# Kernel tuning notes

Measured on AMD Instinct MI355X. Metric: run time of the kernel, lower is better.

Reference implementation:

```python
import jax, jax.numpy as jnp
import numpy as np

B, L, D = 1, 2048, 768
H, DH = 12, 64  # n_heads, d_head (D // H)
LN_EPS = 1e-5
DEN_EPS = 1e-6


def setup_inputs() -> dict:
    key = jax.random.key(0)
    ks = jax.random.split(key, 11)
    s = 0.02
    return {
        "x": jax.random.normal(ks[0], (B, L, D), dtype=jnp.float32),
        "W_qkv": jax.random.normal(ks[1], (D, 3 * D), dtype=jnp.float32) * s,
        "b_qkv": jnp.zeros((3 * D,), dtype=jnp.float32),
        "W_sem": jax.random.normal(ks[2], (D, 2 * D), dtype=jnp.float32) * s,
        "b_sem": jnp.zeros((2 * D,), dtype=jnp.float32),
        "W_ctx": jax.random.normal(ks[3], (D, 2 * D), dtype=jnp.float32) * s,
        "b_ctx": jnp.zeros((2 * D,), dtype=jnp.float32),
        "W_proj": jax.random.normal(ks[4], (D, D), dtype=jnp.float32) * s,
        "b_proj": jnp.zeros((D,), dtype=jnp.float32),
        "ln_g": jnp.ones((D,), dtype=jnp.float32),
        "ln_b": jnp.zeros((D,), dtype=jnp.float32),
    }


def _heads(t):
    # [B,L,D] -> [B,H,L,DH]
    return t.reshape(B, L, H, DH).transpose(0, 2, 1, 3)


def reference(x, W_qkv, b_qkv, W_sem, b_sem, W_ctx, b_ctx, W_proj, b_proj, ln_g, ln_b):
    # LayerNorm
    mu = jnp.mean(x, axis=-1, keepdims=True)
    var = jnp.mean(jnp.square(x - mu), axis=-1, keepdims=True)
    x_norm = (x - mu) * jax.lax.rsqrt(var + LN_EPS) * ln_g + ln_b

    qkv = x_norm @ W_qkv + b_qkv
    q, k, v = jnp.split(qkv, 3, axis=-1)

    # interference gate from raw x
    sem = x @ W_sem + b_sem
    sem_amp = jax.nn.softplus(sem[..., :D])
    sem_phase = sem[..., D:]
    ctx = x @ W_ctx + b_ctx
    ctx_amp = jax.nn.softplus(ctx[..., :D])
    ctx_phase = ctx[..., D:]
    gate = jax.nn.sigmoid(sem_amp * ctx_amp * jnp.cos(sem_phase - ctx_phase))
    k = k * gate

    q_f = jax.nn.elu(_heads(q)) + 1.0  # [B,H,L,DH]
    k_f = jax.nn.elu(_heads(k)) + 1.0
    v_f = _heads(v)

    # causal linear attention: cumsum of kv outer products along L
    kv = jnp.einsum("bhld,bhle->bhlde", k_f, v_f)  # [B,H,L,DH,DH]
    kv_cum = jnp.cumsum(kv, axis=2)
    out_num = jnp.einsum("bhld,bhlde->bhle", q_f, kv_cum)  # [B,H,L,DH]

    k_cum = jnp.cumsum(k_f, axis=2)
    out_den = jnp.sum(q_f * k_cum, axis=-1, keepdims=True) + DEN_EPS

    attn = (out_num / out_den).transpose(0, 2, 1, 3).reshape(B, L, D)
    return attn @ W_proj + b_proj
```

## Files before the change

### kernel.cpp

```cpp
#include <hip/hip_runtime.h>
#include <math.h>

#define LSEQ 2048
#define DMODEL 768
#define NHEAD 12
#define DHEAD 64
#define NCHUNK 32
#define NMERGED 5376

typedef unsigned short ushort_t;
typedef __attribute__((ext_vector_type(8))) short short8;
typedef float float4v __attribute__((ext_vector_type(4)));

__device__ __forceinline__ ushort_t f2b(float f) {
    union { float f; unsigned int u; } v; v.f = f;
    unsigned int u = v.u;
    return (ushort_t)((u + 0x7fffu + ((u >> 16) & 1u)) >> 16);
}
__device__ __forceinline__ float b2f(ushort_t u) {
    union { unsigned int u; float f; } v; v.u = ((unsigned int)u) << 16;
    return v.f;
}

__device__ __forceinline__ void gl_lds16(const ushort_t* g, ushort_t* l) {
    __builtin_amdgcn_global_load_lds(
        (const __attribute__((address_space(1))) unsigned int*)g,
        (__attribute__((address_space(3))) unsigned int*)l, 16, 0, 0);
}

__global__ void ln_kernel(const float* __restrict__ x, const float* __restrict__ g,
                          const float* __restrict__ beta, ushort_t* __restrict__ xn,
                          ushort_t* __restrict__ xb) {
    int row = blockIdx.x;
    int tid = threadIdx.x;
    const float* xr = x + (size_t)row * DMODEL;
    float v0 = xr[tid], v1 = xr[tid + 256], v2 = xr[tid + 512];
    __shared__ float red[4];
    __shared__ float bc;
    float s = v0 + v1 + v2;
#pragma unroll
    for (int o = 32; o > 0; o >>= 1) s += __shfl_down(s, o);
    if ((tid & 63) == 0) red[tid >> 6] = s;
    __syncthreads();
    if (tid == 0) bc = (red[0] + red[1] + red[2] + red[3]) * (1.0f / DMODEL);
    __syncthreads();
    float mu = bc;
    float d0 = v0 - mu, d1 = v1 - mu, d2 = v2 - mu;
    float vs = d0 * d0 + d1 * d1 + d2 * d2;
    __syncthreads();
#pragma unroll
    for (int o = 32; o > 0; o >>= 1) vs += __shfl_down(vs, o);
    if ((tid & 63) == 0) red[tid >> 6] = vs;
    __syncthreads();
    if (tid == 0) bc = rsqrtf((red[0] + red[1] + red[2] + red[3]) * (1.0f / DMODEL) + 1e-5f);
    __syncthreads();
    float r = bc;
    ushort_t* xo = xn + (size_t)row * DMODEL;
    ushort_t* xc = xb + (size_t)row * DMODEL;
    xo[tid]       = f2b(d0 * r * g[tid]       + beta[tid]);
    xo[tid + 256] = f2b(d1 * r * g[tid + 256] + beta[tid + 256]);
    xo[tid + 512] = f2b(d2 * r * g[tid + 512] + beta[tid + 512]);
    xc[tid]       = f2b(v0);
    xc[tid + 256] = f2b(v1);
    xc[tid + 512] = f2b(v2);
}

__global__ void transpose_all_kernel(const float* __restrict__ Wq, const float* __restrict__ Ws,
                                     const float* __restrict__ Wc, ushort_t* __restrict__ Tm,
                                     const float* __restrict__ Wp, ushort_t* __restrict__ Tp) {
    const float* W; ushort_t* Wt; int N;
    switch (blockIdx.z) {
        case 0: W = Wq; Wt = Tm;                        N = 2304; break;
        case 1: W = Ws; Wt = Tm + (size_t)2304 * 768;   N = 1536; break;
        case 2: W = Wc; Wt = Tm + (size_t)3840 * 768;   N = 1536; break;
        default: W = Wp; Wt = Tp;                       N = 768;  break;
    }
    int nbase = blockIdx.x * 32;
    if (nbase >= N) return;
    __shared__ float tile[32][33];
    int tid = threadIdx.x;
    int tr = tid >> 5, tc = tid & 31;
    int kbase = blockIdx.y * 32;
#pragma unroll
    for (int p = 0; p < 4; p++) {
        int r = p * 8 + tr;
        tile[r][tc] = W[(size_t)(kbase + r) * N + nbase + tc];
    }
    __syncthreads();
#pragma unroll
    for (int p = 0; p < 4; p++) {
        int r = p * 8 + tr;
        Wt[(size_t)(nbase + r) * 768 + kbase + tc] = f2b(tile[tc][r]);
    }
}

__global__ __launch_bounds__(256) void gemm_merged_kernel(
    const ushort_t* __restrict__ Axn, const ushort_t* __restrict__ Axb,
    const ushort_t* __restrict__ Bt,
    const float* __restrict__ b_qkv, const float* __restrict__ b_sem,
    const float* __restrict__ b_ctx, float* __restrict__ C,
    ushort_t* __restrict__ vb) {
    const int K = 768, N = NMERGED;
    __shared__ ushort_t As[128 * 32];
    __shared__ ushort_t Bs[128 * 32];
    int tid = threadIdx.x;
    int wave = tid >> 6, lane = tid & 63;
    int wm = (wave >> 1) * 64, wn = (wave & 1) * 64;
    int quad = lane >> 4, l16 = lane & 15;
    int m0 = blockIdx.y * 128, n0 = blockIdx.x * 128;
    const ushort_t* A = (n0 < 2304) ? Axn : Axb;
    const float* bias = (n0 < 2304) ? (b_qkv + n0) : (n0 < 3840 ? (b_sem + n0 - 2304) : (b_ctx + n0 - 3840));

    int r0 = tid >> 2;
    int kc = (tid & 3) * 8;
    const ushort_t* Ag0 = A + (size_t)(m0 + r0) * K + kc;
    const ushort_t* Ag1 = A + (size_t)(m0 + 64 + r0) * K + kc;
    const ushort_t* Bg0 = Bt + (size_t)(n0 + r0) * K + kc;
    const ushort_t* Bg1 = Bt + (size_t)(n0 + 64 + r0) * K + kc;
    ushort_t* Al0 = &As[(wave * 64) * 8];
    ushort_t* Al1 = &As[(256 + wave * 64) * 8];
    ushort_t* Bl0 = &Bs[(wave * 64) * 8];
    ushort_t* Bl1 = &Bs[(256 + wave * 64) * 8];

    float4v acc[4][4];
#pragma unroll
    for (int i = 0; i < 4; i++)
#pragma unroll
        for (int j = 0; j < 4; j++)
#pragma unroll
            for (int r = 0; r < 4; r++) acc[i][j][r] = 0.0f;

    for (int k0 = 0; k0 < K; k0 += 32) {
        gl_lds16(Ag0 + k0, Al0);
        gl_lds16(Ag1 + k0, Al1);
        gl_lds16(Bg0 + k0, Bl0);
        gl_lds16(Bg1 + k0, Bl1);
        __syncthreads();
        short8 af[4], bf[4];
#pragma unroll
        for (int i = 0; i < 4; i++) af[i] = *(const short8*)&As[(wm + i * 16 + l16) * 32 + quad * 8];
#pragma unroll
        for (int j = 0; j < 4; j++) bf[j] = *(const short8*)&Bs[(wn + j * 16 + l16) * 32 + quad * 8];
#pragma unroll
        for (int i = 0; i < 4; i++)
#pragma unroll
            for (int j = 0; j < 4; j++)
                acc[i][j] = __builtin_amdgcn_mfma_f32_16x16x32_bf16(af[i], bf[j], acc[i][j], 0, 0, 0);
        __syncthreads();
    }
    bool is_v = (n0 >= 1536 && n0 < 2304);
#pragma unroll
    for (int i = 0; i < 4; i++) {
#pragma unroll
        for (int j = 0; j < 4; j++) {
            int colb = wn + j * 16 + l16;
            float bv = bias[colb];
#pragma unroll
            for (int r = 0; r < 4; r++) {
                int row = m0 + wm + i * 16 + quad * 4 + r;
                float o = acc[i][j][r] + bv;
                if (is_v) {
                    vb[(size_t)row * DMODEL + (n0 - 1536) + colb] = f2b(o);
                } else {
                    C[(size_t)row * N + n0 + colb] = o;
                }
            }
        }
    }
}

__global__ __launch_bounds__(256) void gemm_64_kernel(
    const ushort_t* __restrict__ A, const ushort_t* __restrict__ Bt,
    const float* __restrict__ bias, float* __restrict__ C,
    int N, int K) {
    __shared__ ushort_t As[64 * 32];
    __shared__ ushort_t Bs[64 * 32];
    int tid = threadIdx.x;
    int wave = tid >> 6, lane = tid & 63;
    int wm = (wave >> 1) * 32, wn = (wave & 1) * 32;
    int quad = lane >> 4, l16 = lane & 15;
    int m0 = blockIdx.y * 64, n0 = blockIdx.x * 64;

    int r0 = tid >> 2;
    int kc = (tid & 3) * 8;
    const ushort_t* Ag = A + (size_t)(m0 + r0) * K + kc;
    const ushort_t* Bg = Bt + (size_t)(n0 + r0) * K + kc;
    ushort_t* Al = &As[(wave * 16) * 32];
    ushort_t* Bl = &Bs[(wave * 16) * 32];

    float4v acc[2][2];
#pragma unroll
    for (int i = 0; i < 2; i++)
#pragma unroll
        for (int j = 0; j < 2; j++)
#pragma unroll
            for (int r = 0; r < 4; r++) acc[i][j][r] = 0.0f;

    for (int k0 = 0; k0 < K; k0 += 32) {
        gl_lds16(Ag + k0, Al);
        gl_lds16(Bg + k0, Bl);
        __syncthreads();
        short8 af[2], bf[2];
#pragma unroll
        for (int i = 0; i < 2; i++) af[i] = *(const short8*)&As[(wm + i * 16 + l16) * 32 + quad * 8];
#pragma unroll
        for (int j = 0; j < 2; j++) bf[j] = *(const short8*)&Bs[(wn + j * 16 + l16) * 32 + quad * 8];
#pragma unroll
        for (int i = 0; i < 2; i++)
#pragma unroll
            for (int j = 0; j < 2; j++)
                acc[i][j] = __builtin_amdgcn_mfma_f32_16x16x32_bf16(af[i], bf[j], acc[i][j], 0, 0, 0);
        __syncthreads();
    }
#pragma unroll
    for (int i = 0; i < 2; i++) {
#pragma unroll
        for (int j = 0; j < 2; j++) {
            int col = n0 + wn + j * 16 + l16;
            float bv = bias[col];
#pragma unroll
            for (int r = 0; r < 4; r++) {
                int row = m0 + wm + i * 16 + quad * 4 + r;
                C[(size_t)row * N + col] = acc[i][j][r] + bv;
            }
        }
    }
}

__device__ __forceinline__ float softplus_f(float x) {
    return (x > 15.f) ? x : log1pf(expf(x));
}

__global__ void gate_feat_kernel(const float* __restrict__ qsc,
                                 ushort_t* __restrict__ qf, ushort_t* __restrict__ kf) {
    int t = blockIdx.x * 256 + threadIdx.x;
    int l = t / 192, d = (t - l * 192) * 4;
    size_t base = (size_t)l * NMERGED;
    float sa[4], sp[4], ca[4], cp[4], q[4], k[4];
    *(float4*)sa = *(const float4*)&qsc[base + 2304 + d];
    *(float4*)sp = *(const float4*)&qsc[base + 3072 + d];
    *(float4*)ca = *(const float4*)&qsc[base + 3840 + d];
    *(float4*)cp = *(const float4*)&qsc[base + 4608 + d];
    *(float4*)q  = *(const float4*)&qsc[base + d];
    *(float4*)k  = *(const float4*)&qsc[base + 768 + d];
    ushort_t qo[4], ko[4];
#pragma unroll
    for (int j = 0; j < 4; j++) {
        float amp = softplus_f(sa[j]) * softplus_f(ca[j]);
        float tt = amp * cosf(sp[j] - cp[j]);
        float gate = 1.0f / (1.0f + expf(-tt));
        float kv = k[j] * gate;
        float qv = q[j];
        qo[j] = f2b((qv > 0.f) ? qv + 1.0f : expf(qv));
        ko[j] = f2b((kv > 0.f) ? kv + 1.0f : expf(kv));
    }
    size_t o = (size_t)l * DMODEL + d;
    *(uint2*)&qf[o] = *(uint2*)qo;
    *(uint2*)&kf[o] = *(uint2*)ko;
}

__global__ __launch_bounds__(256) void chunk_sum_mfma(const ushort_t* __restrict__ kf,
                                                      const ushort_t* __restrict__ vb,
                                                      float* __restrict__ S) {
    int h = blockIdx.x % NHEAD;
    int c = blockIdx.x / NHEAD;
    __shared__ ushort_t Kt[64 * 72];
    __shared__ ushort_t Vt[64 * 72];
    int tid = threadIdx.x;
    const size_t hb = (size_t)h * DHEAD;
#pragma unroll
    for (int it = 0; it < 4; it++) {
        int r = it * 16 + (tid >> 4);
        int cc = (tid & 15) * 4;
        int lg = c * 64 + r;
        ushort_t kt4[4], vt4[4];
        *(uint2*)kt4 = *(const uint2*)&kf[(size_t)lg * DMODEL + hb + cc];
        *(uint2*)vt4 = *(const uint2*)&vb[(size_t)lg * DMODEL + hb + cc];
#pragma unroll
        for (int i2 = 0; i2 < 4; i2++) {
            Kt[(cc + i2) * 72 + r] = kt4[i2];
            Vt[(cc + i2) * 72 + r] = vt4[i2];
        }
    }
    __syncthreads();
    int wave = tid >> 6, lane = tid & 63, quad = lane >> 4, l16 = lane & 15;
    int wm = wave * 16;
    float4v acc[4];
#pragma unroll
    for (int jt = 0; jt < 4; jt++)
#pragma unroll
        for (int r = 0; r < 4; r++) acc[jt][r] = 0.0f;
#pragma unroll
    for (int ks = 0; ks < 2; ks++) {
        short8 af = *(const short8*)&Kt[(wm + l16) * 72 + ks * 32 + quad * 8];
#pragma unroll
        for (int jt = 0; jt < 4; jt++) {
            short8 bf = *(const short8*)&Vt[(jt * 16 + l16) * 72 + ks * 32 + quad * 8];
            acc[jt] = __builtin_amdgcn_mfma_f32_16x16x32_bf16(af, bf, acc[jt], 0, 0, 0);
        }
    }
    float* Sp = S + (size_t)(h * NCHUNK + c) * 4160;
#pragma unroll
    for (int jt = 0; jt < 4; jt++) {
        float4 o;
        o.x = acc[jt][0]; o.y = acc[jt][1]; o.z = acc[jt][2]; o.w = acc[jt][3];
        *(float4*)&Sp[(jt * 16 + l16) * 64 + wm + quad * 4] = o;
    }
    if (tid < 64) {
        float s = 0.f;
#pragma unroll
        for (int g = 0; g < 8; g++) {
            short8 kv8 = *(const short8*)&Kt[tid * 72 + g * 8];
#pragma unroll
            for (int i2 = 0; i2 < 8; i2++) s += b2f(((ushort_t*)&kv8)[i2]);
        }
        Sp[4096 + tid] = s;
    }
}

__global__ void prefix_kernel(const float* __restrict__ S, ushort_t* __restrict__ Pb,
                              float* __restrict__ kpf) {
    int h = blockIdx.x;
    int i = blockIdx.y * 256 + threadIdx.x;
    if (i >= 4160) return;
    float v[NCHUNK];
    size_t base = (size_t)h * NCHUNK * 4160 + i;
#pragma unroll
    for (int c2 = 0; c2 < NCHUNK; c2++) v[c2] = S[base + (size_t)c2 * 4160];
    float run = 0.f;
    if (i < 4096) {
        size_t pb = (size_t)h * NCHUNK * 4096 + i;
#pragma unroll
        for (int c2 = 0; c2 < NCHUNK; c2++) {
            Pb[pb + (size_t)c2 * 4096] = f2b(run);
            run += v[c2];
        }
    } else {
        size_t kb = (size_t)h * NCHUNK * 64 + (i - 4096);
#pragma unroll
        for (int c2 = 0; c2 < NCHUNK; c2++) {
            kpf[kb + (size_t)c2 * 64] = run;
            run += v[c2];
        }
    }
}

__global__ __launch_bounds__(256) void attn_out_mfma(const ushort_t* __restrict__ qf,
                                                     const ushort_t* __restrict__ kf,
                                                     const ushort_t* __restrict__ vb,
                                                     const ushort_t* __restrict__ Pb,
                                                     const float* __restrict__ kpf,
                                                     ushort_t* __restrict__ attn) {
    int h = blockIdx.x % NHEAD;
    int c = blockIdx.x / NHEAD;
    __shared__ ushort_t Qs[64 * 72];
    __shared__ ushort_t Ks[64 * 72];
    __shared__ ushort_t Pt[64 * 72];
    __shared__ ushort_t Vt[64 * 72];
    __shared__ float Sc[64 * 68];
    __shared__ float kpl[64];
    __shared__ float denp[4][64];
    __shared__ float dnl[64];
    int tid = threadIdx.x;
    const size_t hb = (size_t)h * DHEAD;
    const size_t pcb = (size_t)(h * NCHUNK + c);
#pragma unroll
    for (int it = 0; it < 2; it++) {
        int chunk = it * 256 + tid;
        int r = chunk >> 3, c8 = (chunk & 7) * 8;
        int lg = c * 64 + r;
        *(uint4*)&Qs[r * 72 + c8] = *(const uint4*)&qf[(size_t)lg * DMODEL + hb + c8];
        *(uint4*)&Ks[r * 72 + c8] = *(const uint4*)&kf[(size_t)lg * DMODEL + hb + c8];
        *(uint4*)&Pt[r * 72 + c8] = *(const uint4*)&Pb[pcb * 4096 + r * 64 + c8];
    }
#pragma unroll
    for (int it = 0; it < 4; it++) {
        int r = it * 16 + (tid >> 4);
        int cc = (tid & 15) * 4;
        int lg = c * 64 + r;
        ushort_t vt4[4];
        *(uint2*)vt4 = *(const uint2*)&vb[(size_t)lg * DMODEL + hb + cc];
#pragma unroll
        for (int i2 = 0; i2 < 4; i2++) Vt[(cc + i2) * 72 + r] = vt4[i2];
    }
    if (tid < 64) kpl[tid] = kpf[pcb * 64 + tid];
    __syncthreads();
    int wave = tid >> 6, lane = tid & 63, quad = lane >> 4, l16 = lane & 15;
    int wm = wave * 16;
    float4v s_acc[4], n_acc[4];
#pragma unroll
    for (int jt = 0; jt < 4; jt++)
#pragma unroll
        for (int r = 0; r < 4; r++) { s_acc[jt][r] = 0.0f; n_acc[jt][r] = 0.0f; }
#pragma unroll
    for (int ks = 0; ks < 2; ks++) {
        short8 aq = *(const short8*)&Qs[(wm + l16) * 72 + ks * 32 + quad * 8];
#pragma unroll
        for (int jt = 0; jt < 4; jt++) {
            short8 bk = *(const short8*)&Ks[(jt * 16 + l16) * 72 + ks * 32 + quad * 8];
            short8 bp = *(const short8*)&Pt[(jt * 16 + l16) * 72 + ks * 32 + quad * 8];
            s_acc[jt] = __builtin_amdgcn_mfma_f32_16x16x32_bf16(aq, bk, s_acc[jt], 0, 0, 0);
            n_acc[jt] = __builtin_amdgcn_mfma_f32_16x16x32_bf16(aq, bp, n_acc[jt], 0, 0, 0);
        }
    }
#pragma unroll
    for (int jt = 0; jt < 4; jt++)
#pragma unroll
        for (int r = 0; r < 4; r++)
            Sc[(wm + quad * 4 + r) * 68 + jt * 16 + l16] = s_acc[jt][r];
    __syncthreads();
    {
        int l = tid & 63, part = tid >> 6;
        float s = 0.f;
#pragma unroll
        for (int jj = 0; jj < 16; jj++) {
            int j = part * 16 + jj;
            float v = Sc[l * 68 + j];
            s += (j <= l) ? v : 0.f;
        }
#pragma unroll
        for (int dd = 0; dd < 16; dd++) {
            int d = part * 16 + dd;
            s += b2f(Qs[l * 72 + d]) * kpl[d];
        }
        denp[part][l] = s;
    }
    __syncthreads();
    if (tid < 64) dnl[tid] = denp[0][tid] + denp[1][tid] + denp[2][tid] + denp[3][tid] + 1e-6f;
    __syncthreads();
#pragma unroll
    for (int ks = 0; ks < 2; ks++) {
        int m = wm + l16;
        float sv[8];
        *(float4*)&sv[0] = *(const float4*)&Sc[m * 68 + ks * 32 + quad * 8];
        *(float4*)&sv[4] = *(const float4*)&Sc[m * 68 + ks * 32 + quad * 8 + 4];
        ushort_t am[8];
#pragma unroll
        for (int i2 = 0; i2 < 8; i2++) {
            int j = ks * 32 + quad * 8 + i2;
            am[i2] = (j <= m) ? f2b(sv[i2]) : (ushort_t)0;
        }
        short8 af = *(short8*)am;
#pragma unroll
        for (int jt = 0; jt < 4; jt++) {
            short8 bv = *(const short8*)&Vt[(jt * 16 + l16) * 72 + ks * 32 + quad * 8];
            n_acc[jt] = __builtin_amdgcn_mfma_f32_16x16x32_bf16(af, bv, n_acc[jt], 0, 0, 0);
        }
    }
#pragma unroll
    for (int jt = 0; jt < 4; jt++) {
        int e = jt * 16 + l16;
#pragma unroll
        for (int r = 0; r < 4; r++) {
            int l = wm + quad * 4 + r;
            float o = n_acc[jt][r] / dnl[l];
            attn[(size_t)(c * 64 + l) * DMODEL + hb + e] = f2b(o);
        }
    }
}

extern "C" void kernel_launch(void* const* d_in, const int* in_sizes, int n_in,
                              void* d_out, int out_size, void* d_ws, size_t ws_size,
                              hipStream_t stream) {
    const float* x      = (const float*)d_in[0];
    const float* W_qkv  = (const float*)d_in[1];
    const float* b_qkv  = (const float*)d_in[2];
    const float* W_sem  = (const float*)d_in[3];
    const float* b_sem  = (const float*)d_in[4];
    const float* W_ctx  = (const float*)d_in[5];
    const float* b_ctx  = (const float*)d_in[6];
    const float* W_proj = (const float*)d_in[7];
    const float* b_proj = (const float*)d_in[8];
    const float* ln_g   = (const float*)d_in[9];
    const float* ln_b   = (const float*)d_in[10];
    float* out = (float*)d_out;
    float* ws  = (float*)d_ws;

    ushort_t* Wt_merged = (ushort_t*)(ws);
    ushort_t* Wt_proj   = (ushort_t*)(ws + 2064384);
    ushort_t* xb        = (ushort_t*)(ws + 2359296);
    ushort_t* xnb       = (ushort_t*)(ws + 3145728);
    float*    qsc       = ws + 3932160;
    ushort_t* vb        = (ushort_t*)(ws + 14942208);
    ushort_t* qf        = (ushort_t*)(ws + 2359296);
    ushort_t* kf        = (ushort_t*)(ws + 3145728);
    float*    S         = ws;
    ushort_t* Pb        = (ushort_t*)(ws + 3932160);
    float*    kpf       = ws + 4718592;
    ushort_t* attnb     = (ushort_t*)(ws);

    ln_kernel<<<LSEQ, 256, 0, stream>>>(x, ln_g, ln_b, xnb, xb);
    transpose_all_kernel<<<dim3(72, 24, 4), 256, 0, stream>>>(W_qkv, W_sem, W_ctx, Wt_merged,
                                                              W_proj, Wt_proj);

    gemm_merged_kernel<<<dim3(NMERGED / 128, LSEQ / 128), 256, 0, stream>>>(
        xnb, xb, Wt_merged, b_qkv, b_sem, b_ctx, qsc, vb);

    gate_feat_kernel<<<(LSEQ * DMODEL / 4) / 256, 256, 0, stream>>>(qsc, qf, kf);
    chunk_sum_mfma<<<NHEAD * NCHUNK, 256, 0, stream>>>(kf, vb, S);
    prefix_kernel<<<dim3(NHEAD, 17), 256, 0, stream>>>(S, Pb, kpf);
    attn_out_mfma<<<NHEAD * NCHUNK, 256, 0, stream>>>(qf, kf, vb, Pb, kpf, attnb);

    gemm_64_kernel<<<dim3(768 / 64, LSEQ / 64), 256, 0, stream>>>(attnb, Wt_proj, b_proj, out, 768, 768);
}
```

Measured before the change: 163.4 us.

## Fuse LN with weight transpose, widen GEMM K-tile with swizzled LDS, store bf16 intermediates

Merges the LayerNorm and weight-transpose kernels into one launch, saving a kernel launch and letting the two run concurrently. Both MFMA GEMMs now stage a 64-wide K slice per iteration, halving the number of barriers. LDS rows are XOR-swizzled to avoid bank conflicts. The merged GEMM writes its large intermediate (q, k, sem, ctx) as bf16 instead of fp32, halving the store and reload traffic for the gate kernel at the cost of lower precision in the gate inputs.

```diff
diff --git a/kernel.cpp b/kernel.cpp
--- a/kernel.cpp
+++ b/kernel.cpp
@@ -28,69 +28,73 @@
         (__attribute__((address_space(3))) unsigned int*)l, 16, 0, 0);
 }
 
-__global__ void ln_kernel(const float* __restrict__ x, const float* __restrict__ g,
-                          const float* __restrict__ beta, ushort_t* __restrict__ xn,
-                          ushort_t* __restrict__ xb) {
-    int row = blockIdx.x;
-    int tid = threadIdx.x;
-    const float* xr = x + (size_t)row * DMODEL;
-    float v0 = xr[tid], v1 = xr[tid + 256], v2 = xr[tid + 512];
+__global__ void pre_kernel(const float* __restrict__ x, const float* __restrict__ g,
+                           const float* __restrict__ beta, ushort_t* __restrict__ xn,
+                           ushort_t* __restrict__ xb,
+                           const float* __restrict__ Wq, const float* __restrict__ Ws,
+                           const float* __restrict__ Wc, ushort_t* __restrict__ Tm,
+                           const float* __restrict__ Wp, ushort_t* __restrict__ Tp) {
     __shared__ float red[4];
     __shared__ float bc;
-    float s = v0 + v1 + v2;
-#pragma unroll
-    for (int o = 32; o > 0; o >>= 1) s += __shfl_down(s, o);
-    if ((tid & 63) == 0) red[tid >> 6] = s;
-    __syncthreads();
-    if (tid == 0) bc = (red[0] + red[1] + red[2] + red[3]) * (1.0f / DMODEL);
-    __syncthreads();
-    float mu = bc;
-    float d0 = v0 - mu, d1 = v1 - mu, d2 = v2 - mu;
-    float vs = d0 * d0 + d1 * d1 + d2 * d2;
-    __syncthreads();
-#pragma unroll
-    for (int o = 32; o > 0; o >>= 1) vs += __shfl_down(vs, o);
-    if ((tid & 63) == 0) red[tid >> 6] = vs;
-    __syncthreads();
-    if (tid == 0) bc = rsqrtf((red[0] + red[1] + red[2] + red[3]) * (1.0f / DMODEL) + 1e-5f);
-    __syncthreads();
-    float r = bc;
-    ushort_t* xo = xn + (size_t)row * DMODEL;
-    ushort_t* xc = xb + (size_t)row * DMODEL;
-    xo[tid]       = f2b(d0 * r * g[tid]       + beta[tid]);
-    xo[tid + 256] = f2b(d1 * r * g[tid + 256] + beta[tid + 256]);
-    xo[tid + 512] = f2b(d2 * r * g[tid + 512] + beta[tid + 512]);
-    xc[tid]       = f2b(v0);
-    xc[tid + 256] = f2b(v1);
-    xc[tid + 512] = f2b(v2);
-}
-
-__global__ void transpose_all_kernel(const float* __restrict__ Wq, const float* __restrict__ Ws,
-                                     const float* __restrict__ Wc, ushort_t* __restrict__ Tm,
-                                     const float* __restrict__ Wp, ushort_t* __restrict__ Tp) {
-    const float* W; ushort_t* Wt; int N;
-    switch (blockIdx.z) {
-        case 0: W = Wq; Wt = Tm;                        N = 2304; break;
-        case 1: W = Ws; Wt = Tm + (size_t)2304 * 768;   N = 1536; break;
-        case 2: W = Wc; Wt = Tm + (size_t)3840 * 768;   N = 1536; break;
-        default: W = Wp; Wt = Tp;                       N = 768;  break;
-    }
-    int nbase = blockIdx.x * 32;
-    if (nbase >= N) return;
     __shared__ float tile[32][33];
     int tid = threadIdx.x;
-    int tr = tid >> 5, tc = tid & 31;
-    int kbase = blockIdx.y * 32;
-#pragma unroll
-    for (int p = 0; p < 4; p++) {
-        int r = p * 8 + tr;
-        tile[r][tc] = W[(size_t)(kbase + r) * N + nbase + tc];
-    }
-    __syncthreads();
-#pragma unroll
-    for (int p = 0; p < 4; p++) {
-        int r = p * 8 + tr;
-        Wt[(size_t)(nbase + r) * 768 + kbase + tc] = f2b(tile[tc][r]);
+    if (blockIdx.x < 2048) {
+        int row = blockIdx.x;
+        const float* xr = x + (size_t)row * DMODEL;
+        float v0 = xr[tid], v1 = xr[tid + 256], v2 = xr[tid + 512];
+        float s = v0 + v1 + v2;
+#pragma unroll
+        for (int o = 32; o > 0; o >>= 1) s += __shfl_down(s, o);
+        if ((tid & 63) == 0) red[tid >> 6] = s;
+        __syncthreads();
+        if (tid == 0) bc = (red[0] + red[1] + red[2] + red[3]) * (1.0f / DMODEL);
+        __syncthreads();
+        float mu = bc;
+        float d0 = v0 - mu, d1 = v1 - mu, d2 = v2 - mu;
+        float vs = d0 * d0 + d1 * d1 + d2 * d2;
+        __syncthreads();
+#pragma unroll
+        for (int o = 32; o > 0; o >>= 1) vs += __shfl_down(vs, o);
+        if ((tid & 63) == 0) red[tid >> 6] = vs;
+        __syncthreads();
+        if (tid == 0) bc = rsqrtf((red[0] + red[1] + red[2] + red[3]) * (1.0f / DMODEL) + 1e-5f);
+        __syncthreads();
+        float r = bc;
+        ushort_t* xo = xn + (size_t)row * DMODEL;
+        ushort_t* xc = xb + (size_t)row * DMODEL;
+        xo[tid]       = f2b(d0 * r * g[tid]       + beta[tid]);
+        xo[tid + 256] = f2b(d1 * r * g[tid + 256] + beta[tid + 256]);
+        xo[tid + 512] = f2b(d2 * r * g[tid + 512] + beta[tid + 512]);
+        xc[tid]       = f2b(v0);
+        xc[tid + 256] = f2b(v1);
+        xc[tid + 512] = f2b(v2);
+    } else {
+        int bid = blockIdx.x - 2048;
+        int nb = bid % 72;
+        int kb = (bid / 72) % 24;
+        int zb = bid / (72 * 24);
+        const float* W; ushort_t* Wt; int N;
+        switch (zb) {
+            case 0: W = Wq; Wt = Tm;                        N = 2304; break;
+            case 1: W = Ws; Wt = Tm + (size_t)2304 * 768;   N = 1536; break;
+            case 2: W = Wc; Wt = Tm + (size_t)3840 * 768;   N = 1536; break;
+            default: W = Wp; Wt = Tp;                       N = 768;  break;
+        }
+        int nbase = nb * 32;
+        if (nbase >= N) return;
+        int tr = tid >> 5, tc = tid & 31;
+        int kbase = kb * 32;
+#pragma unroll
+        for (int p = 0; p < 4; p++) {
+            int r = p * 8 + tr;
+            tile[r][tc] = W[(size_t)(kbase + r) * N + nbase + tc];
+        }
+        __syncthreads();
+#pragma unroll
+        for (int p = 0; p < 4; p++) {
+            int r = p * 8 + tr;
+            Wt[(size_t)(nbase + r) * 768 + kbase + tc] = f2b(tile[tc][r]);
+        }
     }
 }
 
@@ -98,11 +102,11 @@
     const ushort_t* __restrict__ Axn, const ushort_t* __restrict__ Axb,
     const ushort_t* __restrict__ Bt,
     const float* __restrict__ b_qkv, const float* __restrict__ b_sem,
-    const float* __restrict__ b_ctx, float* __restrict__ C,
+    const float* __restrict__ b_ctx, ushort_t* __restrict__ Cb,
     ushort_t* __restrict__ vb) {
-    const int K = 768, N = NMERGED;
-    __shared__ ushort_t As[128 * 32];
-    __shared__ ushort_t Bs[128 * 32];
+    const int K = 768;
+    __shared__ ushort_t As[128 * 64];
+    __shared__ ushort_t Bs[128 * 64];
     int tid = threadIdx.x;
     int wave = tid >> 6, lane = tid & 63;
     int wm = (wave >> 1) * 64, wn = (wave & 1) * 64;
@@ -111,16 +115,9 @@
     const ushort_t* A = (n0 < 2304) ? Axn : Axb;
     const float* bias = (n0 < 2304) ? (b_qkv + n0) : (n0 < 3840 ? (b_sem + n0 - 2304) : (b_ctx + n0 - 3840));
 
-    int r0 = tid >> 2;
-    int kc = (tid & 3) * 8;
-    const ushort_t* Ag0 = A + (size_t)(m0 + r0) * K + kc;
-    const ushort_t* Ag1 = A + (size_t)(m0 + 64 + r0) * K + kc;
-    const ushort_t* Bg0 = Bt + (size_t)(n0 + r0) * K + kc;
-    const ushort_t* Bg1 = Bt + (size_t)(n0 + 64 + r0) * K + kc;
-    ushort_t* Al0 = &As[(wave * 64) * 8];
-    ushort_t* Al1 = &As[(256 + wave * 64) * 8];
-    ushort_t* Bl0 = &Bs[(wave * 64) * 8];
-    ushort_t* Bl1 = &Bs[(256 + wave * 64) * 8];
+    int rb = tid >> 3;
+    int c8 = tid & 7;
+    ushort_t* Al = &As[(size_t)(tid >> 6) * 512 * 8 / 8];
 
     float4v acc[4][4];
 #pragma unroll
@@ -130,22 +127,34 @@
 #pragma unroll
             for (int r = 0; r < 4; r++) acc[i][j][r] = 0.0f;
 
-    for (int k0 = 0; k0 < K; k0 += 32) {
-        gl_lds16(Ag0 + k0, Al0);
-        gl_lds16(Ag1 + k0, Al1);
-        gl_lds16(Bg0 + k0, Bl0);
-        gl_lds16(Bg1 + k0, Bl1);
-        __syncthreads();
-        short8 af[4], bf[4];
-#pragma unroll
-        for (int i = 0; i < 4; i++) af[i] = *(const short8*)&As[(wm + i * 16 + l16) * 32 + quad * 8];
-#pragma unroll
-        for (int j = 0; j < 4; j++) bf[j] = *(const short8*)&Bs[(wn + j * 16 + l16) * 32 + quad * 8];
-#pragma unroll
-        for (int i = 0; i < 4; i++)
-#pragma unroll
-            for (int j = 0; j < 4; j++)
-                acc[i][j] = __builtin_amdgcn_mfma_f32_16x16x32_bf16(af[i], bf[j], acc[i][j], 0, 0, 0);
+    for (int k0 = 0; k0 < K; k0 += 64) {
+#pragma unroll
+        for (int p = 0; p < 4; p++) {
+            int r = p * 32 + rb;
+            int kc = (c8 ^ (r & 7)) * 8;
+            gl_lds16(A  + (size_t)(m0 + r) * K + k0 + kc, &As[(p * 256 + wave * 64) * 8]);
+            gl_lds16(Bt + (size_t)(n0 + r) * K + k0 + kc, &Bs[(p * 256 + wave * 64) * 8]);
+        }
+        __syncthreads();
+#pragma unroll
+        for (int ks = 0; ks < 2; ks++) {
+            short8 af[4], bf[4];
+#pragma unroll
+            for (int i = 0; i < 4; i++) {
+                int rr = wm + i * 16 + l16;
+                af[i] = *(const short8*)&As[rr * 64 + (((ks * 4 + quad) ^ (rr & 7)) * 8)];
+            }
+#pragma unroll
+            for (int j = 0; j < 4; j++) {
+                int rr = wn + j * 16 + l16;
+                bf[j] = *(const short8*)&Bs[rr * 64 + (((ks * 4 + quad) ^ (rr & 7)) * 8)];
+            }
+#pragma unroll
+            for (int i = 0; i < 4; i++)
+#pragma unroll
+                for (int j = 0; j < 4; j++)
+                    acc[i][j] = __builtin_amdgcn_mfma_f32_16x16x32_bf16(af[i], bf[j], acc[i][j], 0, 0, 0);
+        }
         __syncthreads();
     }
     bool is_v = (n0 >= 1536 && n0 < 2304);
@@ -158,11 +167,11 @@
 #pragma unroll
             for (int r = 0; r < 4; r++) {
                 int row = m0 + wm + i * 16 + quad * 4 + r;
-                float o = acc[i][j][r] + bv;
+                ushort_t o = f2b(acc[i][j][r] + bv);
                 if (is_v) {
-                    vb[(size_t)row * DMODEL + (n0 - 1536) + colb] = f2b(o);
+                    vb[(size_t)row * DMODEL + (n0 - 1536) + colb] = o;
                 } else {
-                    C[(size_t)row * N + n0 + colb] = o;
+                    Cb[(size_t)row * NMERGED + n0 + colb] = o;
                 }
             }
         }
@@ -173,20 +182,16 @@
     const ushort_t* __restrict__ A, const ushort_t* __restrict__ Bt,
     const float* __restrict__ bias, float* __restrict__ C,
     int N, int K) {
-    __shared__ ushort_t As[64 * 32];
-    __shared__ ushort_t Bs[64 * 32];
+    __shared__ ushort_t As[64 * 64];
+    __shared__ ushort_t Bs[64 * 64];
     int tid = threadIdx.x;
     int wave = tid >> 6, lane = tid & 63;
     int wm = (wave >> 1) * 32, wn = (wave & 1) * 32;
     int quad = lane >> 4, l16 = lane & 15;
     int m0 = blockIdx.y * 64, n0 = blockIdx.x * 64;
 
-    int r0 = tid >> 2;
-    int kc = (tid & 3) * 8;
-    const ushort_t* Ag = A + (size_t)(m0 + r0) * K + kc;
-    const ushort_t* Bg = Bt + (size_t)(n0 + r0) * K + kc;
-    ushort_t* Al = &As[(wave * 16) * 32];
-    ushort_t* Bl = &Bs[(wave * 16) * 32];
+    int rb = tid >> 3;
+    int c8 = tid & 7;
 
     float4v acc[2][2];
 #pragma unroll
@@ -196,20 +201,34 @@
 #pragma unroll
             for (int r = 0; r < 4; r++) acc[i][j][r] = 0.0f;
 
-    for (int k0 = 0; k0 < K; k0 += 32) {
-        gl_lds16(Ag + k0, Al);
-        gl_lds16(Bg + k0, Bl);
-        __syncthreads();
-        short8 af[2], bf[2];
-#pragma unroll
-        for (int i = 0; i < 2; i++) af[i] = *(const short8*)&As[(wm + i * 16 + l16) * 32 + quad * 8];
-#pragma unroll
-        for (int j = 0; j < 2; j++) bf[j] = *(const short8*)&Bs[(wn + j * 16 + l16) * 32 + quad * 8];
-#pragma unroll
-        for (int i = 0; i < 2; i++)
-#pragma unroll
-            for (int j = 0; j < 2; j++)
-                acc[i][j] = __builtin_amdgcn_mfma_f32_16x16x32_bf16(af[i], bf[j], acc[i][j], 0, 0, 0);
+    for (int k0 = 0; k0 < K; k0 += 64) {
+#pragma unroll
+        for (int p = 0; p < 2; p++) {
+            int r = p * 32 + rb;
+            int kc = (c8 ^ (r & 7)) * 8;
+            gl_lds16(A  + (size_t)(m0 + r) * K + k0 + kc, &As[(p * 256 + wave * 64) * 8]);
+            gl_lds16(Bt + (size_t)(n0 + r) * K + k0 + kc, &Bs[(p * 256 + wave * 64) * 8]);
+        }
+        __syncthreads();
+#pragma unroll
+        for (int ks = 0; ks < 2; ks++) {
+            short8 af[2], bf[2];
+#pragma unroll
+            for (int i = 0; i < 2; i++) {
+                int rr = wm + i * 16 + l16;
+                af[i] = *(const short8*)&As[rr * 64 + (((ks * 4 + quad) ^ (rr & 7)) * 8)];
+            }
+#pragma unroll
+            for (int j = 0; j < 2; j++) {
+                int rr = wn + j * 16 + l16;
+                bf[j] = *(const short8*)&Bs[rr * 64 + (((ks * 4 + quad) ^ (rr & 7)) * 8)];
+            }
+#pragma unroll
+            for (int i = 0; i < 2; i++)
+#pragma unroll
+                for (int j = 0; j < 2; j++)
+                    acc[i][j] = __builtin_amdgcn_mfma_f32_16x16x32_bf16(af[i], bf[j], acc[i][j], 0, 0, 0);
+        }
         __syncthreads();
     }
 #pragma unroll
@@ -231,26 +250,26 @@
     return (x > 15.f) ? x : log1pf(expf(x));
 }
 
-__global__ void gate_feat_kernel(const float* __restrict__ qsc,
+__global__ void gate_feat_kernel(const ushort_t* __restrict__ qscb,
                                  ushort_t* __restrict__ qf, ushort_t* __restrict__ kf) {
     int t = blockIdx.x * 256 + threadIdx.x;
     int l = t / 192, d = (t - l * 192) * 4;
     size_t base = (size_t)l * NMERGED;
-    float sa[4], sp[4], ca[4], cp[4], q[4], k[4];
-    *(float4*)sa = *(const float4*)&qsc[base + 2304 + d];
-    *(float4*)sp = *(const float4*)&qsc[base + 3072 + d];
-    *(float4*)ca = *(const float4*)&qsc[base + 3840 + d];
-    *(float4*)cp = *(const float4*)&qsc[base + 4608 + d];
-    *(float4*)q  = *(const float4*)&qsc[base + d];
-    *(float4*)k  = *(const float4*)&qsc[base + 768 + d];
+    ushort_t sa[4], sp[4], ca[4], cp[4], q[4], k[4];
+    *(uint2*)sa = *(const uint2*)&qscb[base + 2304 + d];
+    *(uint2*)sp = *(const uint2*)&qscb[base + 3072 + d];
+    *(uint2*)ca = *(const uint2*)&qscb[base + 3840 + d];
+    *(uint2*)cp = *(const uint2*)&qscb[base + 4608 + d];
+    *(uint2*)q  = *(const uint2*)&qscb[base + d];
+    *(uint2*)k  = *(const uint2*)&qscb[base + 768 + d];
     ushort_t qo[4], ko[4];
 #pragma unroll
     for (int j = 0; j < 4; j++) {
-        float amp = softplus_f(sa[j]) * softplus_f(ca[j]);
-        float tt = amp * cosf(sp[j] - cp[j]);
+        float amp = softplus_f(b2f(sa[j])) * softplus_f(b2f(ca[j]));
+        float tt = amp * cosf(b2f(sp[j]) - b2f(cp[j]));
         float gate = 1.0f / (1.0f + expf(-tt));
-        float kv = k[j] * gate;
-        float qv = q[j];
+        float kv = b2f(k[j]) * gate;
+        float qv = b2f(q[j]);
         qo[j] = f2b((qv > 0.f) ? qv + 1.0f : expf(qv));
         ko[j] = f2b((kv > 0.f) ? kv + 1.0f : expf(kv));
     }
@@ -480,7 +499,7 @@
     ushort_t* Wt_proj   = (ushort_t*)(ws + 2064384);
     ushort_t* xb        = (ushort_t*)(ws + 2359296);
     ushort_t* xnb       = (ushort_t*)(ws + 3145728);
-    float*    qsc       = ws + 3932160;
+    ushort_t* qscb      = (ushort_t*)(ws + 3932160);
     ushort_t* vb        = (ushort_t*)(ws + 14942208);
     ushort_t* qf        = (ushort_t*)(ws + 2359296);
     ushort_t* kf        = (ushort_t*)(ws + 3145728);
@@ -489,14 +508,14 @@
     float*    kpf       = ws + 4718592;
     ushort_t* attnb     = (ushort_t*)(ws);
 
-    ln_kernel<<<LSEQ, 256, 0, stream>>>(x, ln_g, ln_b, xnb, xb);
-    transpose_all_kernel<<<dim3(72, 24, 4), 256, 0, stream>>>(W_qkv, W_sem, W_ctx, Wt_merged,
-                                                              W_proj, Wt_proj);
+    pre_kernel<<<2048 + 72 * 24 * 4, 256, 0, stream>>>(x, ln_g, ln_b, xnb, xb,
+                                                       W_qkv, W_sem, W_ctx, Wt_merged,
+                                                       W_proj, Wt_proj);
 
     gemm_merged_kernel<<<dim3(NMERGED / 128, LSEQ / 128), 256, 0, stream>>>(
-        xnb, xb, Wt_merged, b_qkv, b_sem, b_ctx, qsc, vb);
-
-    gate_feat_kernel<<<(LSEQ * DMODEL / 4) / 256, 256, 0, stream>>>(qsc, qf, kf);
+        xnb, xb, Wt_merged, b_qkv, b_sem, b_ctx, qscb, vb);
+
+    gate_feat_kernel<<<(LSEQ * DMODEL / 4) / 256, 256, 0, stream>>>(qscb, qf, kf);
     chunk_sum_mfma<<<NHEAD * NCHUNK, 256, 0, stream>>>(kf, vb, S);
     prefix_kernel<<<dim3(NHEAD, 17), 256, 0, stream>>>(S, Pb, kpf);
     attn_out_mfma<<<NHEAD * NCHUNK, 256, 0, stream>>>(qf, kf, vb, Pb, kpf, attnb);
```

New measurement: 173.1 us. +5.9%, slower.
